# Kernel optimization log

Hardware: AMD Instinct MI355X
Metric: run time of the kernel (lower is better)

The kernel has to match this reference:

```python
import jax, jax.numpy as jnp
import numpy as np


def setup_inputs() -> dict:
    key = jax.random.key(0)
    x = jax.random.normal(key, (32, 3, 512, 512), dtype=jnp.float32)
    return {"x": x}


def reference(x):
    # Faithful vectorized form of the triple-loop 2x2 block flatten:
    # out[b, c*H*W + i*W + 4*j + 2*r + s] = x[b, c, 2*i + r, 2*j + s]
    B, C, H, W = x.shape
    # [B, C, H//2, 2, W//2, 2] -> (b, c, i, r, j, s)
    y = x.reshape(B, C, H // 2, 2, W // 2, 2)
    # reorder to (b, c, i, j, r, s); flattening (i, j, r, s) yields
    # i*(W//2*4) + j*4 + r*2 + s = i*W + 4*j + 2*r + s, matching the loop offsets
    y = jnp.transpose(y, (0, 1, 2, 4, 3, 5))
    return y.reshape(B, C * H * W)
```

## Files before the change

### kernel.cpp

```cpp
#include <hip/hip_runtime.h>


namespace {
constexpr int B = 32;
constexpr int C = 3;
constexpr int H = 512;
constexpr int W = 512;
constexpr int HALF_H = H / 2;
constexpr int QW = W / 4;
constexpr long long TOTAL_THREADS = (long long)B * C * HALF_H * QW;
}

__global__ __launch_bounds__(256) void flatten2x2_kernel(const float* __restrict__ x,
                                                         float* __restrict__ out) {
    long long t = (long long)blockIdx.x * blockDim.x + threadIdx.x;
    if (t >= TOTAL_THREADS) return;

    int tj = (int)(t % QW);
    long long rest = t / QW;
    int i = (int)(rest % HALF_H);
    int bc = (int)(rest / HALF_H);

    long long plane = (long long)bc * H * W;
    const float4* row0 = (const float4*)(x + plane + (long long)(2 * i) * W);
    const float4* row1 = (const float4*)(x + plane + (long long)(2 * i + 1) * W);

    float4 r0 = row0[tj];
    float4 r1 = row1[tj];

    float4* o = (float4*)(out + plane + (long long)i * (2 * W) + (long long)8 * tj);
    o[0] = make_float4(r0.x, r0.y, r1.x, r1.y);
    o[1] = make_float4(r0.z, r0.w, r1.z, r1.w);
}

extern "C" void kernel_launch(void* const* d_in, const int* in_sizes, int n_in,
                              void* d_out, int out_size, void* d_ws, size_t ws_size,
                              hipStream_t stream) {
    const float* x = (const float*)d_in[0];
    float* out = (float*)d_out;

    const int block = 256;
    const int grid = (int)((TOTAL_THREADS + block - 1) / block);
    flatten2x2_kernel<<<grid, block, 0, stream>>>(x, out);
}
```

Measured before the change: 176.3 us.

## Stage 2x2 block reorder through LDS with fully coalesced float4 loads and stores

Each block now loads a contiguous 4096-float tile (each wave takes one pair of rows) into shared memory with coalesced float4 loads. It then reads float2 pairs from the two rows and writes contiguous float4 outputs. Previously each thread wrote two float4s at a stride of 8 floats and read two separate rows, so a wave's stores interleaved. The change adds a block-wide barrier and LDS traffic in return for simpler indexing and fully contiguous per-wave access.

```diff
diff --git a/kernel.cpp b/kernel.cpp
--- a/kernel.cpp
+++ b/kernel.cpp
@@ -6,31 +6,38 @@
 constexpr int C = 3;
 constexpr int H = 512;
 constexpr int W = 512;
-constexpr int HALF_H = H / 2;
-constexpr int QW = W / 4;
-constexpr long long TOTAL_THREADS = (long long)B * C * HALF_H * QW;
+constexpr int TILE_FLOATS = 4096;
+constexpr int NTILES = B * C * H * W / TILE_FLOATS;
 }
 
-__global__ __launch_bounds__(256) void flatten2x2_kernel(const float* __restrict__ x,
-                                                         float* __restrict__ out) {
-    long long t = (long long)blockIdx.x * blockDim.x + threadIdx.x;
-    if (t >= TOTAL_THREADS) return;
+__global__ __launch_bounds__(256) void flatten2x2_lds(const float* __restrict__ x,
+                                                      float* __restrict__ out) {
+    __shared__ float lds[TILE_FLOATS];
 
-    int tj = (int)(t % QW);
-    long long rest = t / QW;
-    int i = (int)(rest % HALF_H);
-    int bc = (int)(rest / HALF_H);
+    const int tid = threadIdx.x;
+    const int w = tid >> 6;
+    const int lane = tid & 63;
 
-    long long plane = (long long)bc * H * W;
-    const float4* row0 = (const float4*)(x + plane + (long long)(2 * i) * W);
-    const float4* row1 = (const float4*)(x + plane + (long long)(2 * i + 1) * W);
+    const long long tile = (long long)blockIdx.x * TILE_FLOATS;
 
-    float4 r0 = row0[tj];
-    float4 r1 = row1[tj];
+    const float4* __restrict__ src = (const float4*)(x + tile + 1024 * w);
+    float4* ldsv = (float4*)(lds + 1024 * w);
+#pragma unroll
+    for (int m = 0; m < 4; ++m) {
+        ldsv[64 * m + lane] = src[64 * m + lane];
+    }
+    __syncthreads();
 
-    float4* o = (float4*)(out + plane + (long long)i * (2 * W) + (long long)8 * tj);
-    o[0] = make_float4(r0.x, r0.y, r1.x, r1.y);
-    o[1] = make_float4(r0.z, r0.w, r1.z, r1.w);
+    const float2* r0 = (const float2*)(lds + 1024 * w);
+    const float2* r1 = (const float2*)(lds + 1024 * w + 512);
+    float4* __restrict__ dst = (float4*)(out + tile + 1024 * w);
+#pragma unroll
+    for (int m = 0; m < 4; ++m) {
+        const int j = 64 * m + lane;
+        const float2 a = r0[j];
+        const float2 b = r1[j];
+        dst[j] = make_float4(a.x, a.y, b.x, b.y);
+    }
 }
 
 extern "C" void kernel_launch(void* const* d_in, const int* in_sizes, int n_in,
@@ -39,7 +46,5 @@
     const float* x = (const float*)d_in[0];
     float* out = (float*)d_out;
 
-    const int block = 256;
-    const int grid = (int)((TOTAL_THREADS + block - 1) / block);
-    flatten2x2_kernel<<<grid, block, 0, stream>>>(x, out);
+    flatten2x2_lds<<<NTILES, 256, 0, stream>>>(x, out);
 }
```

Result: no change. 173.0 us (-1.9%).
